# Kernel tuning notes

Measured on AMD Instinct MI355X. Metric: run time of the kernel, lower is better.

## Reference

```python
import jax, jax.numpy as jnp
import numpy as np

N, C, G = 262144, 256, 1024
R = C // 4  # reduction bottleneck


def _linear_w(key, out_dim, in_dim):
    # torch.nn.Linear default init: U(-1/sqrt(in), 1/sqrt(in)), weight shape [out, in]
    bound = 1.0 / np.sqrt(in_dim)
    return jax.random.uniform(key, (out_dim, in_dim), jnp.float32, -bound, bound)


def setup_inputs() -> dict:
    key = jax.random.key(0)
    ks = jax.random.split(key, 8)
    return {
        "x": jax.random.normal(ks[0], (N, C), jnp.float32),
        "glb_w1": _linear_w(ks[1], R, C),
        "glb_a": jnp.full((1,), 0.25, jnp.float32),   # PReLU param (default init 0.25)
        "glb_w2": _linear_w(ks[2], C, R),
        "local_w1": _linear_w(ks[3], R, C),
        "local_a": jnp.full((1,), 0.25, jnp.float32),
        "local_w2": _linear_w(ks[4], C, R),
        "attn_w1": _linear_w(ks[5], R, C),
        "attn_a": jnp.full((1,), 0.25, jnp.float32),
        "attn_w2": _linear_w(ks[6], C, R),
        "batch_idx": jnp.sort(jax.random.randint(ks[7], (N,), 0, G)),
        "num_graphs": G,
    }


def _mlp(h, w1, a, w2):
    # Linear(no bias) -> PReLU -> Linear(no bias)
    z = jnp.einsum('nc,rc->nr', h, w1)
    z = jnp.where(z >= 0, z, a * z)
    return jnp.einsum('nr,cr->nc', z, w2)


def reference(x, glb_w1, glb_a, glb_w2, local_w1, local_a, local_w2,
              attn_w1, attn_a, attn_w2, batch_idx, num_graphs):
    g = _mlp(x, glb_w1, glb_a, glb_w2)                                  # [N, C]
    seg_sum = jax.ops.segment_sum(g, batch_idx, num_segments=num_graphs)  # [G, C]
    cnt = jax.ops.segment_sum(jnp.ones((x.shape[0], 1), x.dtype), batch_idx,
                              num_segments=num_graphs)                  # [G, 1]
    seg_mean = seg_sum / jnp.maximum(cnt, 1.0)  # scatter_mean (0 for empty graphs)
    x_glb = seg_mean[batch_idx]                                          # gather back [N, C]
    loc = _mlp(x, local_w1, local_a, local_w2)                           # [N, C]
    attn = _mlp(loc + x_glb, attn_w1, attn_a, attn_w2)
    return jax.nn.sigmoid(attn)
```

## Files before the change

### kernel.cpp

```cpp
#include <hip/hip_runtime.h>

typedef unsigned short u16;
typedef __attribute__((ext_vector_type(8))) short short8;
typedef __attribute__((ext_vector_type(4))) float f32x4;
typedef __attribute__((ext_vector_type(4))) unsigned short u16x4;
typedef __attribute__((ext_vector_type(2))) unsigned u32x2;

#define NN 262144
#define CC 256
#define RR 64
#define GG 1024

#define SWZ(b, n) ((b) ^ (((n) & 7) << 4))


static __device__ __forceinline__ u16 f2bf(float f) {
  unsigned u = __builtin_bit_cast(unsigned, f);
  u += 0x7fffu + ((u >> 16) & 1u);
  return (u16)(u >> 16);
}

static __device__ __forceinline__ unsigned cvt_pk_bf16(float lo, float hi) {
  unsigned r;
  asm("v_cvt_pk_bf16_f32 %0, %1, %2" : "=v"(r) : "v"(lo), "v"(hi));
  return r;
}

static __device__ __forceinline__ void lgkm0() {
  __asm__ volatile("s_waitcnt lgkmcnt(0)" ::: "memory");
}

#define MFMA16(a, b, c) __builtin_amdgcn_mfma_f32_16x16x32_bf16((a), (b), (c), 0, 0, 0)

__global__ void k_cvt(const float* __restrict__ a0, const float* __restrict__ a1,
                      const float* __restrict__ a2, const float* __restrict__ a3,
                      const float* __restrict__ a4, const float* __restrict__ a5,
                      u16* __restrict__ dst) {
  int m = blockIdx.x >> 4;
  const float* s = (m == 0) ? a0 : (m == 1) ? a1 : (m == 2) ? a2
                 : (m == 3) ? a3 : (m == 4) ? a4 : a5;
  int off = (((blockIdx.x & 15) << 8) | threadIdx.x) << 2;
  f32x4 v = *(const f32x4*)(s + off);
  u16x4 p;
  p[0] = f2bf(v[0]); p[1] = f2bf(v[1]); p[2] = f2bf(v[2]); p[3] = f2bf(v[3]);
  *(u16x4*)(dst + m * 16384 + off) = p;
}


__global__ __launch_bounds__(256)
__attribute__((amdgpu_waves_per_eu(5, 5))) void k_glb(
    const float* __restrict__ x, const u16* __restrict__ wbf,
    const int* __restrict__ bidx, const float* __restrict__ pa,
    float* __restrict__ seg, int* __restrict__ cnt) {
  __shared__ __align__(16) char smem[32768];
  const int tid = threadIdx.x;
  const int wave = tid >> 6, lane = tid & 63;
  const int low = lane & 15, quad = lane >> 4;
  const int node0 = blockIdx.x << 6;
  const float alpha = pa[0];
  const u16* w1 = wbf;
  const u16* w2 = wbf + 16384;

  int myb_lb = (tid < 64) ? bidx[node0 + tid] : 0;

  const float* xsrc = x + (size_t)node0 * CC;
#pragma unroll
  for (int k = 0; k < 16; k++) {
    int f = k * 1024 + tid * 4;
    f32x4 v = *(const f32x4*)(xsrc + f);
    int node = f >> 8;
    u32x2 p;
    p[0] = cvt_pk_bf16(v[0], v[1]);
    p[1] = cvt_pk_bf16(v[2], v[3]);
    *(u32x2*)(smem + SWZ(node * 512 + (f & 255) * 2, node)) = p;
  }
  __syncthreads();

  f32x4 z[4] = {};
  const u16* w1p = w1 + (wave * 16 + low) * CC;
#pragma unroll
  for (int ks = 0; ks < 8; ks++) {
    short8 wa = *(const short8*)(w1p + ks * 32 + quad * 8);
#pragma unroll
    for (int nt = 0; nt < 4; nt++) {
      int node = nt * 16 + low;
      short8 xf = *(const short8*)(smem + SWZ(node * 512 + ks * 64 + quad * 16, node));
      z[nt] = MFMA16(wa, xf, z[nt]);
    }
  }
  __syncthreads();

  if (tid < 64) ((int*)(smem + 25600))[tid] = myb_lb;
#pragma unroll
  for (int nt = 0; nt < 4; nt++) {
    float v0 = z[nt][0], v1 = z[nt][1], v2 = z[nt][2], v3 = z[nt][3];
    v0 = v0 >= 0.f ? v0 : alpha * v0;
    v1 = v1 >= 0.f ? v1 : alpha * v1;
    v2 = v2 >= 0.f ? v2 : alpha * v2;
    v3 = v3 >= 0.f ? v3 : alpha * v3;
    int node = nt * 16 + low;
    u32x2 p;
    p[0] = cvt_pk_bf16(v0, v1);
    p[1] = cvt_pk_bf16(v2, v3);
    *(u32x2*)(smem + SWZ(node * 128 + wave * 32 + quad * 8, node)) = p;
  }
  __syncthreads();

  const int* lbp = (const int*)(smem + 25600);

  if (lane == 0) {
    int base = wave * 16;
    int cur = lbp[base], rl = 0;
#pragma unroll
    for (int n = 0; n < 16; n++) {
      int b = lbp[base + n];
      if (b != cur) { atomicAdd(cnt + cur, rl); rl = 0; cur = b; }
      rl++;
    }
    atomicAdd(cnt + cur, rl);
  }

  float* slab = (float*)(smem + 8192 + wave * 4352);
#pragma unroll
  for (int nt = 0; nt < 4; nt++) {
    int node = nt * 16 + low;
    f32x4 g[4] = {};
#pragma unroll
    for (int ks2 = 0; ks2 < 2; ks2++) {
      short8 zf = *(const short8*)(smem + SWZ(node * 128 + ks2 * 64 + quad * 16, node));
#pragma unroll
      for (int mt = 0; mt < 4; mt++) {
        short8 wa = *(const short8*)(w2 + (wave * 64 + mt * 16 + low) * RR + ks2 * 32 + quad * 8);
        g[mt] = MFMA16(wa, zf, g[mt]);
      }
    }
#pragma unroll
    for (int mt = 0; mt < 4; mt++)
      *(f32x4*)(slab + low * 68 + mt * 16 + quad * 4) = g[mt];
    lgkm0();
    float acc = 0.f;
    int cur = lbp[nt * 16];
#pragma unroll
    for (int n = 0; n < 16; n++) {
      int b = lbp[nt * 16 + n];
      if (b != cur) {
        atomicAdd(seg + (size_t)cur * CC + wave * 64 + lane, acc);
        acc = 0.f; cur = b;
      }
      acc += slab[n * 68 + lane];
    }
    atomicAdd(seg + (size_t)cur * CC + wave * 64 + lane, acc);
    lgkm0();
  }
}

#define ZBOFF 32768
__global__ __launch_bounds__(256)
__attribute__((amdgpu_waves_per_eu(4, 4))) void k_attn(
    const float* __restrict__ x, const u16* __restrict__ wbf,
    const int* __restrict__ bidx, const float* __restrict__ seg,
    const int* __restrict__ cnt,
    const float* __restrict__ pal, const float* __restrict__ paa,
    float* __restrict__ out) {
  __shared__ __align__(16) char smem[40960];
  const int tid = threadIdx.x;
  const int wave = tid >> 6, lane = tid & 63;
  const int low = lane & 15, quad = lane >> 4;
  const int node0 = blockIdx.x << 6;
  const float al = pal[0], aa = paa[0];
  const u16* w1l = wbf + 2 * 16384;
  const u16* w2l = wbf + 3 * 16384;
  const u16* w1a = wbf + 4 * 16384;
  const u16* w2a = wbf + 5 * 16384;

  int bb[4];
#pragma unroll
  for (int nt = 0; nt < 4; nt++) bb[nt] = bidx[node0 + nt * 16 + low];
  int cc[4];
#pragma unroll
  for (int nt = 0; nt < 4; nt++) cc[nt] = cnt[bb[nt]];

  const float* xsrc = x + (size_t)node0 * CC;
#pragma unroll
  for (int k = 0; k < 16; k++) {
    int f = k * 1024 + tid * 4;
    f32x4 v = *(const f32x4*)(xsrc + f);
    int node = f >> 8;
    u32x2 p;
    p[0] = cvt_pk_bf16(v[0], v[1]);
    p[1] = cvt_pk_bf16(v[2], v[3]);
    *(u32x2*)(smem + SWZ(node * 512 + (f & 255) * 2, node)) = p;
  }
  __syncthreads();

  f32x4 z[4] = {};
  const u16* w1p = w1l + (wave * 16 + low) * CC;
#pragma unroll
  for (int ks = 0; ks < 8; ks++) {
    short8 wa = *(const short8*)(w1p + ks * 32 + quad * 8);
#pragma unroll
    for (int nt = 0; nt < 4; nt++) {
      int node = nt * 16 + low;
      short8 xf = *(const short8*)(smem + SWZ(node * 512 + ks * 64 + quad * 16, node));
      z[nt] = MFMA16(wa, xf, z[nt]);
    }
  }
#pragma unroll
  for (int nt = 0; nt < 4; nt++) {
    float v0 = z[nt][0], v1 = z[nt][1], v2 = z[nt][2], v3 = z[nt][3];
    v0 = v0 >= 0.f ? v0 : al * v0;
    v1 = v1 >= 0.f ? v1 : al * v1;
    v2 = v2 >= 0.f ? v2 : al * v2;
    v3 = v3 >= 0.f ? v3 : al * v3;
    int node = nt * 16 + low;
    u32x2 p;
    p[0] = cvt_pk_bf16(v0, v1);
    p[1] = cvt_pk_bf16(v2, v3);
    *(u32x2*)(smem + ZBOFF + SWZ(node * 128 + wave * 32 + quad * 8, node)) = p;
  }
  __syncthreads();

#pragma unroll
  for (int nt = 0; nt < 4; nt++) {
    int node = nt * 16 + low;
    f32x4 loc[4] = {};
#pragma unroll
    for (int ks2 = 0; ks2 < 2; ks2++) {
      short8 zf = *(const short8*)(smem + ZBOFF + SWZ(node * 128 + ks2 * 64 + quad * 16, node));
#pragma unroll
      for (int mt = 0; mt < 4; mt++) {
        short8 wa = *(const short8*)(w2l + (wave * 64 + mt * 16 + low) * RR + ks2 * 32 + quad * 8);
        loc[mt] = MFMA16(wa, zf, loc[mt]);
      }
    }
    const float* srow = seg + (size_t)bb[nt] * CC + wave * 64;
    float inv = (cc[nt] > 0) ? __builtin_amdgcn_rcpf((float)cc[nt]) : 0.0f;
#pragma unroll
    for (int mt = 0; mt < 4; mt++) {
      f32x4 sv = *(const f32x4*)(srow + mt * 16 + quad * 4);
      u32x2 p;
      p[0] = cvt_pk_bf16(fmaf(sv[0], inv, loc[mt][0]),
                         fmaf(sv[1], inv, loc[mt][1]));
      p[1] = cvt_pk_bf16(fmaf(sv[2], inv, loc[mt][2]),
                         fmaf(sv[3], inv, loc[mt][3]));
      *(u32x2*)(smem + SWZ(node * 512 + wave * 128 + mt * 32 + quad * 8, node)) = p;
    }
  }
  __syncthreads();

  f32x4 z2[4] = {};
  const u16* w1pa = w1a + (wave * 16 + low) * CC;
#pragma unroll
  for (int ks = 0; ks < 8; ks++) {
    short8 wa = *(const short8*)(w1pa + ks * 32 + quad * 8);
#pragma unroll
    for (int nt = 0; nt < 4; nt++) {
      int node = nt * 16 + low;
      short8 hf = *(const short8*)(smem + SWZ(node * 512 + ks * 64 + quad * 16, node));
      z2[nt] = MFMA16(wa, hf, z2[nt]);
    }
  }
#pragma unroll
  for (int nt = 0; nt < 4; nt++) {
    float v0 = z2[nt][0], v1 = z2[nt][1], v2 = z2[nt][2], v3 = z2[nt][3];
    v0 = v0 >= 0.f ? v0 : aa * v0;
    v1 = v1 >= 0.f ? v1 : aa * v1;
    v2 = v2 >= 0.f ? v2 : aa * v2;
    v3 = v3 >= 0.f ? v3 : aa * v3;
    int node = nt * 16 + low;
    u32x2 p;
    p[0] = cvt_pk_bf16(v0, v1);
    p[1] = cvt_pk_bf16(v2, v3);
    *(u32x2*)(smem + ZBOFF + SWZ(node * 128 + wave * 32 + quad * 8, node)) = p;
  }
  __syncthreads();

  float* slab = (float*)(smem + wave * 4352);
#pragma unroll
  for (int nt = 0; nt < 4; nt++) {
    int node = nt * 16 + low;
    f32x4 o[4] = {};
#pragma unroll
    for (int ks2 = 0; ks2 < 2; ks2++) {
      short8 zf = *(const short8*)(smem + ZBOFF + SWZ(node * 128 + ks2 * 64 + quad * 16, node));
#pragma unroll
      for (int mt = 0; mt < 4; mt++) {
        short8 wa = *(const short8*)(w2a + (wave * 64 + mt * 16 + low) * RR + ks2 * 32 + quad * 8);
        o[mt] = MFMA16(wa, zf, o[mt]);
      }
    }
#pragma unroll
    for (int mt = 0; mt < 4; mt++) {
#pragma unroll
      for (int i = 0; i < 4; i++)
        o[mt][i] = __builtin_amdgcn_rcpf(1.0f + __expf(-o[mt][i]));
      *(f32x4*)(slab + low * 68 + mt * 16 + quad * 4) = o[mt];
    }
    lgkm0();
#pragma unroll
    for (int n = 0; n < 16; n++)
      out[(size_t)(node0 + nt * 16 + n) * CC + wave * 64 + lane] = slab[n * 68 + lane];
    lgkm0();
  }
}

extern "C" void kernel_launch(void* const* d_in, const int* in_sizes, int n_in,
                              void* d_out, int out_size, void* d_ws, size_t ws_size,
                              hipStream_t stream) {
  (void)in_sizes; (void)n_in; (void)out_size; (void)ws_size;
  const float* x   = (const float*)d_in[0];
  const float* w1g = (const float*)d_in[1];
  const float* ag  = (const float*)d_in[2];
  const float* w2g = (const float*)d_in[3];
  const float* w1l = (const float*)d_in[4];
  const float* al  = (const float*)d_in[5];
  const float* w2l = (const float*)d_in[6];
  const float* w1a = (const float*)d_in[7];
  const float* aa  = (const float*)d_in[8];
  const float* w2a = (const float*)d_in[9];
  const int* bidx  = (const int*)d_in[10];
  float* out = (float*)d_out;

  u16* wbf   = (u16*)d_ws;
  float* seg = (float*)((char*)d_ws + 196608);
  int* cnt   = (int*)((char*)d_ws + 196608 + 1048576);

  hipMemsetAsync(seg, 0, 1048576 + 4096, stream);
  k_cvt<<<96, 256, 0, stream>>>(w1g, w2g, w1l, w2l, w1a, w2a, wbf);
  k_glb<<<NN / 64, 256, 0, stream>>>(x, wbf, bidx, ag, seg, cnt);
  k_attn<<<NN / 64, 256, 0, stream>>>(x, wbf, bidx, seg, cnt, al, aa, out);
}
```

Measured before the change: 666.2 us.

## Halve node tile per block, raise occupancy, fuse memset into prep kernel

Each block now handles 32 nodes instead of 64, and LDS use drops to 20 KB so both main kernels can target 8 waves per EU instead of 4–5. The separate memset is folded into the weight-conversion kernel. Batch indices are broadcast with shuffles instead of going through LDS, and the count run-length pass moves earlier. The output slab transpose in the attention kernel is removed in favour of direct strided float4 stores, trading coalescing for less LDS traffic and fewer syncs.

Result: slower. 683.8 us (+2.6%).

```diff
diff --git a/kernel.cpp b/kernel.cpp
--- a/kernel.cpp
+++ b/kernel.cpp
@@ -12,6 +12,7 @@
 #define GG 1024
 
 #define SWZ(b, n) ((b) ^ (((n) & 7) << 4))
+#define SSWZ(b, r) ((b) ^ (((r) & 7) << 4))
 
 
 static __device__ __forceinline__ u16 f2bf(float f) {
@@ -32,40 +33,47 @@
 
 #define MFMA16(a, b, c) __builtin_amdgcn_mfma_f32_16x16x32_bf16((a), (b), (c), 0, 0, 0)
 
-__global__ void k_cvt(const float* __restrict__ a0, const float* __restrict__ a1,
-                      const float* __restrict__ a2, const float* __restrict__ a3,
-                      const float* __restrict__ a4, const float* __restrict__ a5,
-                      u16* __restrict__ dst) {
-  int m = blockIdx.x >> 4;
-  const float* s = (m == 0) ? a0 : (m == 1) ? a1 : (m == 2) ? a2
-                 : (m == 3) ? a3 : (m == 4) ? a4 : a5;
-  int off = (((blockIdx.x & 15) << 8) | threadIdx.x) << 2;
-  f32x4 v = *(const f32x4*)(s + off);
-  u16x4 p;
-  p[0] = f2bf(v[0]); p[1] = f2bf(v[1]); p[2] = f2bf(v[2]); p[3] = f2bf(v[3]);
-  *(u16x4*)(dst + m * 16384 + off) = p;
-}
-
+__global__ void k_prep(const float* __restrict__ a0, const float* __restrict__ a1,
+                       const float* __restrict__ a2, const float* __restrict__ a3,
+                       const float* __restrict__ a4, const float* __restrict__ a5,
+                       u16* __restrict__ dst, float* __restrict__ zbase) {
+  int bid = blockIdx.x;
+  if (bid < 96) {
+    int m = bid >> 4;
+    const float* s = (m == 0) ? a0 : (m == 1) ? a1 : (m == 2) ? a2
+                   : (m == 3) ? a3 : (m == 4) ? a4 : a5;
+    int off = (((bid & 15) << 8) | threadIdx.x) << 2;
+    f32x4 v = *(const f32x4*)(s + off);
+    u16x4 p;
+    p[0] = f2bf(v[0]); p[1] = f2bf(v[1]); p[2] = f2bf(v[2]); p[3] = f2bf(v[3]);
+    *(u16x4*)(dst + m * 16384 + off) = p;
+  } else {
+    int idx = (bid - 96) * 256 + threadIdx.x;
+    ((f32x4*)zbase)[idx] = (f32x4){0.f, 0.f, 0.f, 0.f};
+  }
+}
+
+#define ZBOFF 16384
 
 __global__ __launch_bounds__(256)
-__attribute__((amdgpu_waves_per_eu(5, 5))) void k_glb(
+__attribute__((amdgpu_waves_per_eu(8, 8))) void k_glb(
     const float* __restrict__ x, const u16* __restrict__ wbf,
     const int* __restrict__ bidx, const float* __restrict__ pa,
     float* __restrict__ seg, int* __restrict__ cnt) {
-  __shared__ __align__(16) char smem[32768];
+  __shared__ __align__(16) char smem[20480];
   const int tid = threadIdx.x;
   const int wave = tid >> 6, lane = tid & 63;
   const int low = lane & 15, quad = lane >> 4;
-  const int node0 = blockIdx.x << 6;
+  const int node0 = blockIdx.x << 5;
   const float alpha = pa[0];
   const u16* w1 = wbf;
   const u16* w2 = wbf + 16384;
 
-  int myb_lb = (tid < 64) ? bidx[node0 + tid] : 0;
+  const int lbv = bidx[node0 + (lane & 31)];
 
   const float* xsrc = x + (size_t)node0 * CC;
 #pragma unroll
-  for (int k = 0; k < 16; k++) {
+  for (int k = 0; k < 8; k++) {
     int f = k * 1024 + tid * 4;
     f32x4 v = *(const f32x4*)(xsrc + f);
     int node = f >> 8;
@@ -74,25 +82,33 @@
     p[1] = cvt_pk_bf16(v[2], v[3]);
     *(u32x2*)(smem + SWZ(node * 512 + (f & 255) * 2, node)) = p;
   }
-  __syncthreads();
-
-  f32x4 z[4] = {};
+
+  if (wave == 0) {
+    int cur = __shfl(lbv, 0), rl = 0;
+#pragma unroll
+    for (int n = 0; n < 32; n++) {
+      int b = __shfl(lbv, n);
+      if (b != cur) { if (lane == 0) atomicAdd(cnt + cur, rl); rl = 0; cur = b; }
+      rl++;
+    }
+    if (lane == 0) atomicAdd(cnt + cur, rl);
+  }
+  __syncthreads();
+
+  f32x4 z[2] = {};
   const u16* w1p = w1 + (wave * 16 + low) * CC;
 #pragma unroll
   for (int ks = 0; ks < 8; ks++) {
     short8 wa = *(const short8*)(w1p + ks * 32 + quad * 8);
 #pragma unroll
-    for (int nt = 0; nt < 4; nt++) {
+    for (int nt = 0; nt < 2; nt++) {
       int node = nt * 16 + low;
       short8 xf = *(const short8*)(smem + SWZ(node * 512 + ks * 64 + quad * 16, node));
       z[nt] = MFMA16(wa, xf, z[nt]);
     }
   }
-  __syncthreads();
-
-  if (tid < 64) ((int*)(smem + 25600))[tid] = myb_lb;
-#pragma unroll
-  for (int nt = 0; nt < 4; nt++) {
+#pragma unroll
+  for (int nt = 0; nt < 2; nt++) {
     float v0 = z[nt][0], v1 = z[nt][1], v2 = z[nt][2], v3 = z[nt][3];
     v0 = v0 >= 0.f ? v0 : alpha * v0;
     v1 = v1 >= 0.f ? v1 : alpha * v1;
@@ -102,32 +118,18 @@
     u32x2 p;
     p[0] = cvt_pk_bf16(v0, v1);
     p[1] = cvt_pk_bf16(v2, v3);
-    *(u32x2*)(smem + SWZ(node * 128 + wave * 32 + quad * 8, node)) = p;
-  }
-  __syncthreads();
-
-  const int* lbp = (const int*)(smem + 25600);
-
-  if (lane == 0) {
-    int base = wave * 16;
-    int cur = lbp[base], rl = 0;
-#pragma unroll
-    for (int n = 0; n < 16; n++) {
-      int b = lbp[base + n];
-      if (b != cur) { atomicAdd(cnt + cur, rl); rl = 0; cur = b; }
-      rl++;
-    }
-    atomicAdd(cnt + cur, rl);
-  }
-
-  float* slab = (float*)(smem + 8192 + wave * 4352);
-#pragma unroll
-  for (int nt = 0; nt < 4; nt++) {
+    *(u32x2*)(smem + ZBOFF + SWZ(node * 128 + wave * 32 + quad * 8, node)) = p;
+  }
+  __syncthreads();
+
+  char* slab = smem + wave * 4096;
+#pragma unroll
+  for (int nt = 0; nt < 2; nt++) {
     int node = nt * 16 + low;
     f32x4 g[4] = {};
 #pragma unroll
     for (int ks2 = 0; ks2 < 2; ks2++) {
-      short8 zf = *(const short8*)(smem + SWZ(node * 128 + ks2 * 64 + quad * 16, node));
+      short8 zf = *(const short8*)(smem + ZBOFF + SWZ(node * 128 + ks2 * 64 + quad * 16, node));
 #pragma unroll
       for (int mt = 0; mt < 4; mt++) {
         short8 wa = *(const short8*)(w2 + (wave * 64 + mt * 16 + low) * RR + ks2 * 32 + quad * 8);
@@ -136,53 +138,51 @@
     }
 #pragma unroll
     for (int mt = 0; mt < 4; mt++)
-      *(f32x4*)(slab + low * 68 + mt * 16 + quad * 4) = g[mt];
+      *(f32x4*)(slab + SSWZ(low * 256 + mt * 64 + quad * 16, low)) = g[mt];
     lgkm0();
     float acc = 0.f;
-    int cur = lbp[nt * 16];
+    int cur = __shfl(lbv, nt * 16);
 #pragma unroll
     for (int n = 0; n < 16; n++) {
-      int b = lbp[nt * 16 + n];
+      int b = __shfl(lbv, nt * 16 + n);
       if (b != cur) {
         atomicAdd(seg + (size_t)cur * CC + wave * 64 + lane, acc);
         acc = 0.f; cur = b;
       }
-      acc += slab[n * 68 + lane];
+      acc += *(const float*)(slab + SSWZ(n * 256 + lane * 4, n));
     }
     atomicAdd(seg + (size_t)cur * CC + wave * 64 + lane, acc);
     lgkm0();
   }
 }
 
-#define ZBOFF 32768
 __global__ __launch_bounds__(256)
-__attribute__((amdgpu_waves_per_eu(4, 4))) void k_attn(
+__attribute__((amdgpu_waves_per_eu(8, 8))) void k_attn(
     const float* __restrict__ x, const u16* __restrict__ wbf,
     const int* __restrict__ bidx, const float* __restrict__ seg,
     const int* __restrict__ cnt,
     const float* __restrict__ pal, const float* __restrict__ paa,
     float* __restrict__ out) {
-  __shared__ __align__(16) char smem[40960];
+  __shared__ __align__(16) char smem[20480];
   const int tid = threadIdx.x;
   const int wave = tid >> 6, lane = tid & 63;
   const int low = lane & 15, quad = lane >> 4;
-  const int node0 = blockIdx.x << 6;
+  const int node0 = blockIdx.x << 5;
   const float al = pal[0], aa = paa[0];
   const u16* w1l = wbf + 2 * 16384;
   const u16* w2l = wbf + 3 * 16384;
   const u16* w1a = wbf + 4 * 16384;
   const u16* w2a = wbf + 5 * 16384;
 
-  int bb[4];
-#pragma unroll
-  for (int nt = 0; nt < 4; nt++) bb[nt] = bidx[node0 + nt * 16 + low];
-  int cc[4];
-#pragma unroll
-  for (int nt = 0; nt < 4; nt++) cc[nt] = cnt[bb[nt]];
+  int bb[2], cc[2];
+#pragma unroll
+  for (int nt = 0; nt < 2; nt++) bb[nt] = bidx[node0 + nt * 16 + low];
+#pragma unroll
+  for (int nt = 0; nt < 2; nt++) cc[nt] = cnt[bb[nt]];
 
   const float* xsrc = x + (size_t)node0 * CC;
 #pragma unroll
-  for (int k = 0; k < 16; k++) {
+  for (int k = 0; k < 8; k++) {
     int f = k * 1024 + tid * 4;
     f32x4 v = *(const f32x4*)(xsrc + f);
     int node = f >> 8;
@@ -193,20 +193,20 @@
   }
   __syncthreads();
 
-  f32x4 z[4] = {};
+  f32x4 z[2] = {};
   const u16* w1p = w1l + (wave * 16 + low) * CC;
 #pragma unroll
   for (int ks = 0; ks < 8; ks++) {
     short8 wa = *(const short8*)(w1p + ks * 32 + quad * 8);
 #pragma unroll
-    for (int nt = 0; nt < 4; nt++) {
+    for (int nt = 0; nt < 2; nt++) {
       int node = nt * 16 + low;
       short8 xf = *(const short8*)(smem + SWZ(node * 512 + ks * 64 + quad * 16, node));
       z[nt] = MFMA16(wa, xf, z[nt]);
     }
   }
 #pragma unroll
-  for (int nt = 0; nt < 4; nt++) {
+  for (int nt = 0; nt < 2; nt++) {
     float v0 = z[nt][0], v1 = z[nt][1], v2 = z[nt][2], v3 = z[nt][3];
     v0 = v0 >= 0.f ? v0 : al * v0;
     v1 = v1 >= 0.f ? v1 : al * v1;
@@ -221,7 +221,7 @@
   __syncthreads();
 
 #pragma unroll
-  for (int nt = 0; nt < 4; nt++) {
+  for (int nt = 0; nt < 2; nt++) {
     int node = nt * 16 + low;
     f32x4 loc[4] = {};
 #pragma unroll
@@ -248,20 +248,20 @@
   }
   __syncthreads();
 
-  f32x4 z2[4] = {};
+  f32x4 z2[2] = {};
   const u16* w1pa = w1a + (wave * 16 + low) * CC;
 #pragma unroll
   for (int ks = 0; ks < 8; ks++) {
     short8 wa = *(const short8*)(w1pa + ks * 32 + quad * 8);
 #pragma unroll
-    for (int nt = 0; nt < 4; nt++) {
+    for (int nt = 0; nt < 2; nt++) {
       int node = nt * 16 + low;
       short8 hf = *(const short8*)(smem + SWZ(node * 512 + ks * 64 + quad * 16, node));
       z2[nt] = MFMA16(wa, hf, z2[nt]);
     }
   }
 #pragma unroll
-  for (int nt = 0; nt < 4; nt++) {
+  for (int nt = 0; nt < 2; nt++) {
     float v0 = z2[nt][0], v1 = z2[nt][1], v2 = z2[nt][2], v3 = z2[nt][3];
     v0 = v0 >= 0.f ? v0 : aa * v0;
     v1 = v1 >= 0.f ? v1 : aa * v1;
@@ -275,9 +275,8 @@
   }
   __syncthreads();
 
-  float* slab = (float*)(smem + wave * 4352);
-#pragma unroll
-  for (int nt = 0; nt < 4; nt++) {
+#pragma unroll
+  for (int nt = 0; nt < 2; nt++) {
     int node = nt * 16 + low;
     f32x4 o[4] = {};
 #pragma unroll
@@ -289,18 +288,14 @@
         o[mt] = MFMA16(wa, zf, o[mt]);
       }
     }
+    float* orow = out + (size_t)(node0 + node) * CC + wave * 64;
 #pragma unroll
     for (int mt = 0; mt < 4; mt++) {
 #pragma unroll
       for (int i = 0; i < 4; i++)
         o[mt][i] = __builtin_amdgcn_rcpf(1.0f + __expf(-o[mt][i]));
-      *(f32x4*)(slab + low * 68 + mt * 16 + quad * 4) = o[mt];
-    }
-    lgkm0();
-#pragma unroll
-    for (int n = 0; n < 16; n++)
-      out[(size_t)(node0 + nt * 16 + n) * CC + wave * 64 + lane] = slab[n * 68 + lane];
-    lgkm0();
+      *(f32x4*)(orow + mt * 16 + quad * 4) = o[mt];
+    }
   }
 }
 
@@ -325,8 +320,7 @@
   float* seg = (float*)((char*)d_ws + 196608);
   int* cnt   = (int*)((char*)d_ws + 196608 + 1048576);
 
-  hipMemsetAsync(seg, 0, 1048576 + 4096, stream);
-  k_cvt<<<96, 256, 0, stream>>>(w1g, w2g, w1l, w2l, w1a, w2a, wbf);
-  k_glb<<<NN / 64, 256, 0, stream>>>(x, wbf, bidx, ag, seg, cnt);
-  k_attn<<<NN / 64, 256, 0, stream>>>(x, wbf, bidx, seg, cnt, al, aa, out);
-}
+  k_prep<<<353, 256, 0, stream>>>(w1g, w2g, w1l, w2l, w1a, w2a, wbf, seg);
+  k_glb<<<NN / 32, 256, 0, stream>>>(x, wbf, bidx, ag, seg, cnt);
+  k_attn<<<NN / 32, 256, 0, stream>>>(x, wbf, bidx, seg, cnt, al, aa, out);
+}
```
